# Kernel tuning notes

Measured on AMD Instinct MI355X. Metric: run time of the kernel, lower is better.

The kernel has to match this reference:

```python
import jax, jax.numpy as jnp
import numpy as np

N, E, IN_DIM, HID = 50000, 800000, 128, 128
HEADS, HEAD_DIM = 4, HID // 4
LN_EPS = 1e-5
NEG_SLOPE = 0.2


def layer_norm(x, g, b):
    m = jnp.mean(x, axis=-1, keepdims=True)
    v = jnp.mean(jnp.square(x - m), axis=-1, keepdims=True)
    return (x - m) / jnp.sqrt(v + LN_EPS) * g + b


def setup_inputs() -> dict:
    key = jax.random.key(0)
    ks = jax.random.split(key, 24)
    s = lambda k, shape, scale=0.05: jax.random.normal(k, shape, dtype=jnp.float32) * scale
    inp = {
        "x": jax.random.normal(ks[0], (N, IN_DIM), dtype=jnp.float32),
        "edge_weight": jax.random.uniform(ks[1], (E,), dtype=jnp.float32),
        # GATConv params
        "gat_w": s(ks[2], (IN_DIM, HID)),          # lin weight (transposed), bias=False in PyG lin
        "att_src": s(ks[3], (HEADS, HEAD_DIM)),
        "att_dst": s(ks[4], (HEADS, HEAD_DIM)),
        "gat_b": s(ks[5], (HID,)),                 # GATConv bias (concat=True -> size heads*out)
        # predictive-coding branch: spectral_norm(Linear) + LayerNorm + ReLU
        "pc_w": s(ks[6], (HID, HID)),
        "pc_b": s(ks[7], (HID,)),
        "pc_g": jnp.ones((HID,), jnp.float32),
        "pc_bb": jnp.zeros((HID,), jnp.float32),
        # MGF branch: Linear -> (Linear + LayerNorm + ReLU)
        "mgf_w": s(ks[8], (HID, HID)),
        "mgf_b": s(ks[9], (HID,)),
        "sym_w": s(ks[10], (HID, HID)),
        "sym_b": s(ks[11], (HID,)),
        "sym_g": jnp.ones((HID,), jnp.float32),
        "sym_bb": jnp.zeros((HID,), jnp.float32),
        # output projection + final norm
        "out_w": s(ks[12], (3 * HID, HID)),
        "out_b": s(ks[13], (HID,)),
        "norm_g": jnp.ones((HID,), jnp.float32),
        "norm_b": jnp.zeros((HID,), jnp.float32),
        # int-typed graph structure (batch is unused by the layer, kept for fidelity)
        "edge_index": jax.random.randint(ks[14], (2, E), 0, N, dtype=jnp.int64),
        "batch": jax.random.randint(ks[15], (N,), 0, 782, dtype=jnp.int64),
    }
    return inp


def gat_conv(x, edge_index, gat_w, att_src, att_dst, gat_b):
    # PyG GATConv (eval mode, dropout off), add_self_loops=True, concat=True
    loops = jnp.arange(N, dtype=edge_index.dtype)
    src = jnp.concatenate([edge_index[0], loops])
    dst = jnp.concatenate([edge_index[1], loops])
    xp = (x @ gat_w).reshape(N, HEADS, HEAD_DIM)          # [N,H,C]
    a_src = jnp.sum(xp * att_src, axis=-1)                 # [N,H]
    a_dst = jnp.sum(xp * att_dst, axis=-1)                 # [N,H]
    e = jax.nn.leaky_relu(a_src[src] + a_dst[dst], NEG_SLOPE)  # [E+N,H]
    # segment softmax over incoming edges of each destination node
    m = jax.ops.segment_max(e, dst, num_segments=N)        # [N,H]
    e_exp = jnp.exp(e - m[dst])
    denom = jax.ops.segment_sum(e_exp, dst, num_segments=N)
    alpha = e_exp / (denom[dst] + 1e-16)                   # [E+N,H]
    msg = xp[src] * alpha[:, :, None]                      # [E+N,H,C]
    out = jax.ops.segment_sum(msg, dst, num_segments=N)    # [N,H,C]
    return out.reshape(N, HID) + gat_b


def reference(x, edge_weight, gat_w, att_src, att_dst, gat_b,
              pc_w, pc_b, pc_g, pc_bb,
              mgf_w, mgf_b, sym_w, sym_b, sym_g, sym_bb,
              out_w, out_b, norm_g, norm_b,
              edge_index, batch):
    h_gat = gat_conv(x, edge_index, gat_w, att_src, att_dst, gat_b)
    feats = [h_gat]
    # predictive coding: spectral-normalized linear -> LN -> ReLU
    sigma = jnp.linalg.norm(pc_w, ord=2)
    h_pred = jax.nn.relu(layer_norm(h_gat @ (pc_w / sigma) + pc_b, pc_g, pc_bb))
    feats.append(h_pred)
    # MGF: mgf_proj then symbiotic (Linear -> LN -> ReLU)
    h_mgf = jax.nn.relu(layer_norm((h_gat @ mgf_w + mgf_b) @ sym_w + sym_b, sym_g, sym_bb))
    feats.append(h_mgf)
    h_comb = jnp.concatenate(feats, axis=-1)               # [N, 3*HID]
    h_out = h_comb @ out_w + out_b
    return layer_norm(h_out, norm_g, norm_b)
```

## Files before the change

kernel.cpp:

```cpp
#include <hip/hip_runtime.h>
#include <cstddef>

#define HID 128
#define NEG_SLOPE 0.2f
#define LN_EPS 1e-5f

typedef float floatx4 __attribute__((ext_vector_type(4)));
typedef short bf16x8 __attribute__((ext_vector_type(8)));
typedef int intx4 __attribute__((ext_vector_type(4)));
typedef unsigned short u16;
typedef unsigned int u32;

#define MFMA(a, b, c) __builtin_amdgcn_mfma_f32_16x16x32_bf16((a), (b), (c), 0, 0, 0)

__device__ __forceinline__ u16 f2bf(float f) {
  union { float f; unsigned u; } v; v.f = f;
  unsigned r = v.u + 0x7FFF + ((v.u >> 16) & 1);
  return (u16)(r >> 16);
}
__device__ __forceinline__ float bf2f(u16 s) {
  union { unsigned u; float f; } v; v.u = ((unsigned)s) << 16;
  return v.f;
}

__global__ void build_G_zero(const float* __restrict__ W, float* __restrict__ G,
                             int* __restrict__ cnt, int N) {
  const int b = blockIdx.x;
  if (b < HID) {
    int i = b, j = threadIdx.x;
    float s = 0.f;
    for (int k = 0; k < HID; ++k) s = fmaf(W[k*HID + i], W[k*HID + j], s);
    G[i*HID + j] = s;
  } else {
    int i = (b - HID) * 128 + threadIdx.x;
    if (i < N) cnt[i] = 0;
  }
}

__global__ void mat_sq(const float* __restrict__ A, float* __restrict__ C) {
  int i = blockIdx.x, j = threadIdx.x;
  float s = 0.f;
  for (int k = 0; k < HID; ++k) s = fmaf(A[i*HID + k], A[k*HID + j], s);
  C[i*HID + j] = s;
}

__global__ __launch_bounds__(256) void power_iter_lds(
    const float* __restrict__ H, float* __restrict__ out_inv_sigma) {
  __shared__ __align__(16) float Hl[128 * 132];
  __shared__ __align__(16) float v[132];
  __shared__ float ybuf[256];
  __shared__ float red[8];
  const int tid = threadIdx.x;
  {
    const float4* H4 = (const float4*)H;
    float4* Hl4 = (float4*)Hl;
    #pragma unroll
    for (int idx = tid; idx < 128*32; idx += 256) {
      int r = idx >> 5, c = idx & 31;
      Hl4[r*33 + c] = H4[idx];
    }
  }
  if (tid < 128) v[tid] = 1.0f + 0.001f * (float)tid;
  __syncthreads();
  const int j = tid & 127, half = tid >> 7;
  float rho = 0.f;
  for (int it = 0; it < 20; ++it) {
    const float4* hrow = (const float4*)(Hl + j*132 + half*64);
    const float4* vrow = (const float4*)(v) + half*16;
    float y = 0.f;
    #pragma unroll
    for (int q = 0; q < 16; ++q) {
      float4 hq = hrow[q];
      float4 vq = vrow[q];
      y += hq.x*vq.x + hq.y*vq.y + hq.z*vq.z + hq.w*vq.w;
    }
    ybuf[tid] = y;
    __syncthreads();
    float yj = 0.f, vy = 0.f, yy = 0.f;
    if (tid < 128) {
      yj = ybuf[tid] + ybuf[tid + 128];
      vy = v[tid] * yj;
      yy = yj * yj;
    }
    #pragma unroll
    for (int m = 1; m < 64; m <<= 1) { vy += __shfl_xor(vy, m); yy += __shfl_xor(yy, m); }
    if ((tid & 63) == 0) { red[tid>>6] = vy; red[4 + (tid>>6)] = yy; }
    __syncthreads();
    float vyT = red[0] + red[1] + red[2] + red[3];
    float yyT = red[4] + red[5] + red[6] + red[7];
    rho = vyT;
    if (tid < 128) v[tid] = yj * rsqrtf(yyT);
    __syncthreads();
  }
  if (tid == 0) {
    out_inv_sigma[0] = 1.0f / sqrtf(sqrtf(rho));
  }
}

__global__ void prep_all(const float* __restrict__ pc_w, const float* __restrict__ sigma_inv,
                         const float* __restrict__ mgf_w, const float* __restrict__ mgf_b,
                         const float* __restrict__ sym_w, const float* __restrict__ sym_b,
                         const float* __restrict__ out_w,
                         u16* __restrict__ W1t, u16* __restrict__ W2t,
                         u16* __restrict__ Wot, float* __restrict__ bias2) {
  const int b = blockIdx.x;
  const int j = threadIdx.x;
  if (b < HID) {
    float s = 0.f;
    for (int m = 0; m < HID; ++m) s = fmaf(mgf_w[b*HID + m], sym_w[m*HID + j], s);
    W2t[j*HID + b] = f2bf(s);
  } else if (b == HID) {
    float s = sym_b[j];
    for (int m = 0; m < HID; ++m) s = fmaf(mgf_b[m], sym_w[m*HID + j], s);
    bias2[j] = s;
  } else if (b == HID + 1) {
    float sc = sigma_inv[0];
    for (int k = 0; k < HID; ++k) W1t[j*HID + k] = f2bf(pc_w[k*HID + j] * sc);
  } else {
    int p = b - (HID + 2);
    for (int k = 0; k < HID; ++k)
      Wot[p*HID*HID + j*HID + k] = f2bf(out_w[(size_t)(p*HID + k)*HID + j]);
  }
}

__global__ __launch_bounds__(256) void xp_mfma(
    const float* __restrict__ x, const float* __restrict__ W,
    const float* __restrict__ att_src, const float* __restrict__ att_dst,
    u16* __restrict__ xp, float* __restrict__ a_src, float* __restrict__ a_dst,
    int nrows)
{
  __shared__ u16 Wt[128 * 136];
  const int tid = threadIdx.x;
  {
    const float4* W4 = (const float4*)W;
    #pragma unroll
    for (int i = 0; i < 16; ++i) {
      int i4 = tid + i*256;
      int k = i4 >> 5, n4 = i4 & 31;
      float4 w = W4[i4];
      Wt[(n4*4+0)*136 + k] = f2bf(w.x);
      Wt[(n4*4+1)*136 + k] = f2bf(w.y);
      Wt[(n4*4+2)*136 + k] = f2bf(w.z);
      Wt[(n4*4+3)*136 + k] = f2bf(w.w);
    }
  }
  __syncthreads();
  const int lane = tid & 63, wave = tid >> 6;
  const int lr = lane & 15, lg = lane >> 4;
  const int rowbase = blockIdx.x*128 + wave*32;

  bf16x8 a[2][4];
  #pragma unroll
  for (int rf = 0; rf < 2; ++rf) {
    int row = min(rowbase + rf*16 + lr, nrows-1);
    const float* p = x + (size_t)row*HID + lg*8;
    #pragma unroll
    for (int kc = 0; kc < 4; ++kc) {
      float4 q0 = *(const float4*)(p + kc*32);
      float4 q1 = *(const float4*)(p + kc*32 + 4);
      union { bf16x8 v; u16 s[8]; } u;
      u.s[0]=f2bf(q0.x); u.s[1]=f2bf(q0.y); u.s[2]=f2bf(q0.z); u.s[3]=f2bf(q0.w);
      u.s[4]=f2bf(q1.x); u.s[5]=f2bf(q1.y); u.s[6]=f2bf(q1.z); u.s[7]=f2bf(q1.w);
      a[rf][kc] = u.v;
    }
  }
  floatx4 acc[2][8];
  #pragma unroll
  for (int rf = 0; rf < 2; ++rf)
    #pragma unroll
    for (int cf = 0; cf < 8; ++cf) acc[rf][cf] = (floatx4){0,0,0,0};
  #pragma unroll
  for (int kc = 0; kc < 4; ++kc)
    #pragma unroll
    for (int cf = 0; cf < 8; ++cf) {
      bf16x8 b = *(const bf16x8*)&Wt[(cf*16+lr)*136 + kc*32 + lg*8];
      acc[0][cf] = MFMA(a[0][kc], b, acc[0][cf]);
      acc[1][cf] = MFMA(a[1][kc], b, acc[1][cf]);
    }
  float asv[8], adv[8];
  #pragma unroll
  for (int cf = 0; cf < 8; ++cf) {
    asv[cf] = att_src[cf*16 + lr];
    adv[cf] = att_dst[cf*16 + lr];
  }
  #pragma unroll
  for (int rf = 0; rf < 2; ++rf) {
    #pragma unroll
    for (int j = 0; j < 4; ++j) {
      int row = rowbase + rf*16 + lg*4 + j;
      if (row < nrows) {
        #pragma unroll
        for (int cf = 0; cf < 8; ++cf)
          xp[(size_t)row*HID + cf*16 + lr] = f2bf(acc[rf][cf][j]);
      }
      #pragma unroll
      for (int h = 0; h < 4; ++h) {
        float ps = acc[rf][2*h][j]*asv[2*h] + acc[rf][2*h+1][j]*asv[2*h+1];
        float pd = acc[rf][2*h][j]*adv[2*h] + acc[rf][2*h+1][j]*adv[2*h+1];
        #pragma unroll
        for (int m = 1; m < 16; m <<= 1) { ps += __shfl_xor(ps, m); pd += __shfl_xor(pd, m); }
        if (lr == 0 && row < nrows) {
          a_src[(size_t)row*4 + h] = ps;
          a_dst[(size_t)row*4 + h] = pd;
        }
      }
    }
  }
}

__global__ __launch_bounds__(256) void tail_fused(
    const u16* __restrict__ A,
    const u16* __restrict__ W1t, const float* __restrict__ b1,
    const float* __restrict__ g1, const float* __restrict__ bb1,
    const u16* __restrict__ W2t, const float* __restrict__ b2,
    const float* __restrict__ g2, const float* __restrict__ bb2,
    const u16* __restrict__ Wot,
    const float* __restrict__ out_b,
    const float* __restrict__ norm_g, const float* __restrict__ norm_b,
    float* __restrict__ Cout, int nrows)
{
  __shared__ u16 Wbuf[128 * 136];
  __shared__ u16 T[64 * 136];
  const int tid = threadIdx.x;
  const int lane = tid & 63, wave = tid >> 6;
  const int lr = lane & 15, lg = lane >> 4;
  const int rowbase = blockIdx.x * 64;

  int arow = min(rowbase + wave*16 + lr, nrows-1);
  const u16* ap = A + (size_t)arow*HID + lg*8;
  bf16x8 a0 = *(const bf16x8*)(ap);
  bf16x8 a1 = *(const bf16x8*)(ap + 32);
  bf16x8 a2 = *(const bf16x8*)(ap + 64);
  bf16x8 a3 = *(const bf16x8*)(ap + 96);

  bf16x8 st[8];
  auto loadW = [&](const u16* Wsrc) {
    #pragma unroll
    for (int i = 0; i < 8; ++i)
      st[i] = *(const bf16x8*)(Wsrc + (size_t)(tid + i*256) * 8);
  };
  auto writeW = [&]() {
    #pragma unroll
    for (int i = 0; i < 8; ++i) {
      int c = tid + i*256;
      *(bf16x8*)&Wbuf[(c >> 4)*136 + (c & 15)*8] = st[i];
    }
  };
  auto gemmW = [&](floatx4* acc, bf16x8 x0, bf16x8 x1, bf16x8 x2, bf16x8 x3) {
    #pragma unroll
    for (int cf = 0; cf < 8; ++cf) {
      const u16* wb = &Wbuf[(cf*16+lr)*136 + lg*8];
      acc[cf] = MFMA(x0, *(const bf16x8*)(wb),       acc[cf]);
      acc[cf] = MFMA(x1, *(const bf16x8*)(wb + 32),  acc[cf]);
      acc[cf] = MFMA(x2, *(const bf16x8*)(wb + 64),  acc[cf]);
      acc[cf] = MFMA(x3, *(const bf16x8*)(wb + 96),  acc[cf]);
    }
  };
  auto epiT = [&](floatx4* acc, const float* bias, const float* lng, const float* lnb) {
    #pragma unroll
    for (int j = 0; j < 4; ++j) {
      float vv[8]; float s1 = 0.f, s2 = 0.f;
      #pragma unroll
      for (int cf = 0; cf < 8; ++cf) {
        vv[cf] = acc[cf][j] + bias[cf*16 + lr];
        s1 += vv[cf]; s2 += vv[cf]*vv[cf];
      }
      #pragma unroll
      for (int m = 1; m < 16; m <<= 1) { s1 += __shfl_xor(s1, m); s2 += __shfl_xor(s2, m); }
      float mean = s1 * (1.0f/128.0f);
      float var  = s2 * (1.0f/128.0f) - mean*mean;
      float rstd = rsqrtf(var + LN_EPS);
      int lrow = wave*16 + lg*4 + j;
      #pragma unroll
      for (int cf = 0; cf < 8; ++cf) {
        float o = fmaxf((vv[cf]-mean)*rstd*lng[cf*16+lr] + lnb[cf*16+lr], 0.f);
        T[lrow*136 + cf*16 + lr] = f2bf(o);
      }
    }
  };

  floatx4 accO[8];
  #pragma unroll
  for (int cf = 0; cf < 8; ++cf) accO[cf] = (floatx4){0,0,0,0};

  loadW(W1t);
  writeW(); __syncthreads();
  loadW(Wot + (size_t)1*HID*HID);
  {
    floatx4 accT[8];
    #pragma unroll
    for (int cf = 0; cf < 8; ++cf) accT[cf] = (floatx4){0,0,0,0};
    gemmW(accT, a0, a1, a2, a3);
    epiT(accT, b1, g1, bb1);
  }
  __syncthreads();
  writeW(); __syncthreads();
  loadW(W2t);
  {
    const u16* tp = &T[(wave*16 + lr)*136 + lg*8];
    bf16x8 t0 = *(const bf16x8*)(tp);
    bf16x8 t1 = *(const bf16x8*)(tp + 32);
    bf16x8 t2 = *(const bf16x8*)(tp + 64);
    bf16x8 t3 = *(const bf16x8*)(tp + 96);
    gemmW(accO, t0, t1, t2, t3);
  }
  __syncthreads();
  writeW(); __syncthreads();
  loadW(Wot + (size_t)2*HID*HID);
  {
    floatx4 accT[8];
    #pragma unroll
    for (int cf = 0; cf < 8; ++cf) accT[cf] = (floatx4){0,0,0,0};
    gemmW(accT, a0, a1, a2, a3);
    epiT(accT, b2, g2, bb2);
  }
  __syncthreads();
  writeW(); __syncthreads();
  loadW(Wot);
  {
    const u16* tp = &T[(wave*16 + lr)*136 + lg*8];
    bf16x8 t0 = *(const bf16x8*)(tp);
    bf16x8 t1 = *(const bf16x8*)(tp + 32);
    bf16x8 t2 = *(const bf16x8*)(tp + 64);
    bf16x8 t3 = *(const bf16x8*)(tp + 96);
    gemmW(accO, t0, t1, t2, t3);
  }
  __syncthreads();
  writeW(); __syncthreads();
  gemmW(accO, a0, a1, a2, a3);

  #pragma unroll
  for (int j = 0; j < 4; ++j) {
    float vv[8]; float s1 = 0.f, s2 = 0.f;
    #pragma unroll
    for (int cf = 0; cf < 8; ++cf) {
      vv[cf] = accO[cf][j] + out_b[cf*16 + lr];
      s1 += vv[cf]; s2 += vv[cf]*vv[cf];
    }
    #pragma unroll
    for (int m = 1; m < 16; m <<= 1) { s1 += __shfl_xor(s1, m); s2 += __shfl_xor(s2, m); }
    float mean = s1 * (1.0f/128.0f);
    float var  = s2 * (1.0f/128.0f) - mean*mean;
    float rstd = rsqrtf(var + LN_EPS);
    int row = rowbase + wave*16 + lg*4 + j;
    if (row < nrows) {
      #pragma unroll
      for (int cf = 0; cf < 8; ++cf)
        Cout[(size_t)row*HID + cf*16 + lr] = (vv[cf]-mean)*rstd*norm_g[cf*16+lr] + norm_b[cf*16+lr];
    }
  }
}

__global__ __launch_bounds__(256) void hist_rank(
    const int* __restrict__ ei, int E, int N,
    int* __restrict__ cnt, int* __restrict__ rank) {
  const int E4 = E >> 2;
  const intx4* dst4 = (const intx4*)(ei + (size_t)E);
  intx4* rank4 = (intx4*)rank;
  const int stride = gridDim.x * 256;
  for (int i4 = blockIdx.x*256 + threadIdx.x; i4 < E4; i4 += stride) {
    intx4 d4 = __builtin_nontemporal_load(&dst4[i4]);
    intx4 r;
    r.x = ((unsigned)d4.x < (unsigned)N) ? atomicAdd(&cnt[d4.x], 1) : 0;
    r.y = ((unsigned)d4.y < (unsigned)N) ? atomicAdd(&cnt[d4.y], 1) : 0;
    r.z = ((unsigned)d4.z < (unsigned)N) ? atomicAdd(&cnt[d4.z], 1) : 0;
    r.w = ((unsigned)d4.w < (unsigned)N) ? atomicAdd(&cnt[d4.w], 1) : 0;
    rank4[i4] = r;
  }
}

__global__ void hist_rank_tail(const int* __restrict__ ei, int E, int N,
                               int* __restrict__ cnt, int* __restrict__ rank) {
  int t = threadIdx.x;
  int E4 = E >> 2;
  int ntail = E & 3;
  if (t < ntail) {
    int idx = (E4 << 2) + t;
    int d = ei[(size_t)E + idx];
    rank[idx] = ((unsigned)d < (unsigned)N) ? atomicAdd(&cnt[d], 1) : 0;
  }
}

__global__ void scan_local(const int* __restrict__ cnt, int* __restrict__ row_ptr,
                           int* __restrict__ blk_tot, int N) {
  __shared__ int sd[1024];
  int tid = threadIdx.x;
  int i = blockIdx.x * 1024 + tid;
  int v = (i < N) ? cnt[i] : 0;
  sd[tid] = v;
  __syncthreads();
  for (int off = 1; off < 1024; off <<= 1) {
    int t = (tid >= off) ? sd[tid - off] : 0;
    __syncthreads();
    sd[tid] += t;
    __syncthreads();
  }
  if (i < N) row_ptr[i] = sd[tid] - v;
  if (tid == 1023) blk_tot[blockIdx.x] = sd[1023];
}

__global__ void scan_apply2(int* __restrict__ row_ptr,
                            const int* __restrict__ blk_tot, int N, int nb) {
  __shared__ int s_off;
  const int tid = threadIdx.x;
  const int bid = blockIdx.x;
  if (tid < 64) {
    int carry = 0;
    for (int base = 0; base < nb; base += 64) {
      int i = base + tid;
      int v = (i < nb) ? blk_tot[i] : 0;
      int inc = v;
      #pragma unroll
      for (int m = 1; m < 64; m <<= 1) {
        int t = __shfl_up(inc, m);
        if (tid >= m) inc += t;
      }
      if (i == bid) s_off = carry + inc - v;
      int tot = __shfl(inc, 63);
      carry += tot;
    }
    if (bid == 0 && tid == 0) row_ptr[N] = carry;
  }
  __syncthreads();
  int i = bid * 1024 + tid;
  if (i < N) row_ptr[i] += s_off;
}

__global__ __launch_bounds__(256) void fill_rank(
    const int* __restrict__ ei, int E, int N,
    const int* __restrict__ row_ptr, const int* __restrict__ rank,
    int* __restrict__ csr_src) {
  const int E4 = E >> 2;
  const intx4* src4v = (const intx4*)ei;
  const intx4* dst4v = (const intx4*)(ei + (size_t)E);
  const intx4* rank4 = (const intx4*)rank;
  const int stride = gridDim.x * 256;
  for (int i4 = blockIdx.x*256 + threadIdx.x; i4 < E4; i4 += stride) {
    intx4 d4 = __builtin_nontemporal_load(&dst4v[i4]);
    intx4 s4 = __builtin_nontemporal_load(&src4v[i4]);
    intx4 r4 = __builtin_nontemporal_load(&rank4[i4]);
    if ((unsigned)d4.x < (unsigned)N && (unsigned)s4.x < (unsigned)N)
      csr_src[row_ptr[d4.x] + r4.x] = s4.x;
    if ((unsigned)d4.y < (unsigned)N && (unsigned)s4.y < (unsigned)N)
      csr_src[row_ptr[d4.y] + r4.y] = s4.y;
    if ((unsigned)d4.z < (unsigned)N && (unsigned)s4.z < (unsigned)N)
      csr_src[row_ptr[d4.z] + r4.z] = s4.z;
    if ((unsigned)d4.w < (unsigned)N && (unsigned)s4.w < (unsigned)N)
      csr_src[row_ptr[d4.w] + r4.w] = s4.w;
  }
}

__global__ void fill_rank_tail(const int* __restrict__ ei, int E, int N,
                               const int* __restrict__ row_ptr, const int* __restrict__ rank,
                               int* __restrict__ csr_src) {
  int t = threadIdx.x;
  int E4 = E >> 2;
  int ntail = E & 3;
  if (t < ntail) {
    int idx = (E4 << 2) + t;
    int d = ei[(size_t)E + idx];
    int s = ei[idx];
    if ((unsigned)d < (unsigned)N && (unsigned)s < (unsigned)N)
      csr_src[row_ptr[d] + rank[idx]] = s;
  }
}

__global__ __launch_bounds__(64) void gat_aggregate(
    const u16* __restrict__ xp, const float* __restrict__ a_src,
    const float* __restrict__ a_dst, const int* __restrict__ row_ptr,
    const int* __restrict__ csr_src, const float* __restrict__ gat_b,
    u16* __restrict__ h_gat, int N)
{
  const int d = blockIdx.x;
  const int lane = threadIdx.x;
  const int hh = lane >> 4;
  const int c0 = lane * 2;
  const int beg = row_ptr[d], end = row_ptr[d+1];

  const float ad = a_dst[(size_t)d*4 + hh];
  float e0 = a_src[(size_t)d*4 + hh] + ad;
  e0 = (e0 > 0.f) ? e0 : NEG_SLOPE * e0;
  float w0 = __expf(e0);
  u32 xv = *(const u32*)(xp + (size_t)d*HID + c0);
  float acc0 = w0 * bf2f((u16)(xv & 0xFFFF));
  float acc1 = w0 * bf2f((u16)(xv >> 16));
  float den = w0;

  int i = beg;
  for (; i + 4 <= end; i += 4) {
    int s0 = csr_src[i+0], s1 = csr_src[i+1], s2 = csr_src[i+2], s3 = csr_src[i+3];
    float eA = a_src[(size_t)s0*4 + hh] + ad;
    float eB = a_src[(size_t)s1*4 + hh] + ad;
    float eC = a_src[(size_t)s2*4 + hh] + ad;
    float eD = a_src[(size_t)s3*4 + hh] + ad;
    eA = (eA > 0.f) ? eA : NEG_SLOPE * eA;
    eB = (eB > 0.f) ? eB : NEG_SLOPE * eB;
    eC = (eC > 0.f) ? eC : NEG_SLOPE * eC;
    eD = (eD > 0.f) ? eD : NEG_SLOPE * eD;
    float wA = __expf(eA), wB = __expf(eB), wC = __expf(eC), wD = __expf(eD);
    u32 xA = *(const u32*)(xp + (size_t)s0*HID + c0);
    u32 xB = *(const u32*)(xp + (size_t)s1*HID + c0);
    u32 xC = *(const u32*)(xp + (size_t)s2*HID + c0);
    u32 xD = *(const u32*)(xp + (size_t)s3*HID + c0);
    acc0 = fmaf(wA, bf2f((u16)(xA & 0xFFFF)), acc0);
    acc1 = fmaf(wA, bf2f((u16)(xA >> 16)),    acc1);
    acc0 = fmaf(wB, bf2f((u16)(xB & 0xFFFF)), acc0);
    acc1 = fmaf(wB, bf2f((u16)(xB >> 16)),    acc1);
    acc0 = fmaf(wC, bf2f((u16)(xC & 0xFFFF)), acc0);
    acc1 = fmaf(wC, bf2f((u16)(xC >> 16)),    acc1);
    acc0 = fmaf(wD, bf2f((u16)(xD & 0xFFFF)), acc0);
    acc1 = fmaf(wD, bf2f((u16)(xD >> 16)),    acc1);
    den += (wA + wB) + (wC + wD);
  }
  for (; i < end; ++i) {
    int s = csr_src[i];
    float e = a_src[(size_t)s*4 + hh] + ad;
    e = (e > 0.f) ? e : NEG_SLOPE * e;
    float w = __expf(e);
    u32 xw = *(const u32*)(xp + (size_t)s*HID + c0);
    acc0 = fmaf(w, bf2f((u16)(xw & 0xFFFF)), acc0);
    acc1 = fmaf(w, bf2f((u16)(xw >> 16)),    acc1);
    den += w;
  }
  float inv = 1.0f / (den + 1e-16f);
  float o0 = acc0 * inv + gat_b[c0];
  float o1 = acc1 * inv + gat_b[c0 + 1];
  u32 pack = (u32)f2bf(o0) | ((u32)f2bf(o1) << 16);
  *(u32*)(h_gat + (size_t)d*HID + c0) = pack;
}

extern "C" void kernel_launch(void* const* d_in, const int* in_sizes, int n_in,
                              void* d_out, int out_size, void* d_ws, size_t ws_size,
                              hipStream_t stream) {
  const float* x       = (const float*)d_in[0];
  const float* gat_w   = (const float*)d_in[2];
  const float* att_src = (const float*)d_in[3];
  const float* att_dst = (const float*)d_in[4];
  const float* gat_b   = (const float*)d_in[5];
  const float* pc_w    = (const float*)d_in[6];
  const float* pc_b    = (const float*)d_in[7];
  const float* pc_g    = (const float*)d_in[8];
  const float* pc_bb   = (const float*)d_in[9];
  const float* mgf_w   = (const float*)d_in[10];
  const float* mgf_b   = (const float*)d_in[11];
  const float* sym_w   = (const float*)d_in[12];
  const float* sym_b   = (const float*)d_in[13];
  const float* sym_g   = (const float*)d_in[14];
  const float* sym_bb  = (const float*)d_in[15];
  const float* out_w   = (const float*)d_in[16];
  const float* out_b   = (const float*)d_in[17];
  const float* norm_g  = (const float*)d_in[18];
  const float* norm_b  = (const float*)d_in[19];
  const int*   ei      = (const int*)d_in[20];

  const int N = in_sizes[0] / HID;
  const int E = in_sizes[1];
  const int NB = (N + 1023) / 1024;
  const int NZB = (N + 127) / 128;

  char* ws = (char*)d_ws;
  size_t off = 0;
  auto alloc = [&](size_t bytes) -> void* {
    void* p = ws + off;
    off += (bytes + 255) & ~(size_t)255;
    return p;
  };
  u16*   xp       = (u16*)alloc((size_t)N * HID * 2);
  u16*   h_gat    = (u16*)alloc((size_t)N * HID * 2);
  float* a_src    = (float*)alloc((size_t)N * 4 * 4);
  float* a_dst    = (float*)alloc((size_t)N * 4 * 4);
  int*   cnt      = (int*)alloc((size_t)N * 4);
  int*   row_ptr  = (int*)alloc((size_t)(N + 1) * 4);
  int*   erank    = (int*)alloc((size_t)E * 4);
  int*   blk_tot  = (int*)alloc(256 * 4);
  int*   csr_src  = (int*)alloc((size_t)E * 4);
  float* G        = (float*)alloc(HID * HID * 4);
  float* Hm       = (float*)alloc(HID * HID * 4);
  float* bias2    = (float*)alloc(HID * 4);
  float* sigma_inv= (float*)alloc(256);
  u16*   W1t      = (u16*)alloc(HID * HID * 2);
  u16*   W2t      = (u16*)alloc(HID * HID * 2);
  u16*   Wot      = (u16*)alloc(3 * HID * HID * 2);

  const int ntiles = (N + 127) / 128;
  const int ntiles64 = (N + 63) / 64;

  build_G_zero<<<HID + NZB, HID, 0, stream>>>(pc_w, G, cnt, N);
  mat_sq<<<HID, HID, 0, stream>>>(G, Hm);
  power_iter_lds<<<1, 256, 0, stream>>>(Hm, sigma_inv);

  prep_all<<<HID + 5, HID, 0, stream>>>(pc_w, sigma_inv, mgf_w, mgf_b, sym_w, sym_b,
                                        out_w, W1t, W2t, Wot, bias2);

  xp_mfma<<<ntiles, 256, 0, stream>>>(x, gat_w, att_src, att_dst, xp, a_src, a_dst, N);

  hist_rank<<<1024, 256, 0, stream>>>(ei, E, N, cnt, erank);
  if (E & 3) hist_rank_tail<<<1, 64, 0, stream>>>(ei, E, N, cnt, erank);
  scan_local<<<NB, 1024, 0, stream>>>(cnt, row_ptr, blk_tot, N);
  scan_apply2<<<NB, 1024, 0, stream>>>(row_ptr, blk_tot, N, NB);
  fill_rank<<<1024, 256, 0, stream>>>(ei, E, N, row_ptr, erank, csr_src);
  if (E & 3) fill_rank_tail<<<1, 64, 0, stream>>>(ei, E, N, row_ptr, erank, csr_src);

  gat_aggregate<<<N, 64, 0, stream>>>(xp, a_src, a_dst, row_ptr, csr_src,
                                      gat_b, h_gat, N);

  tail_fused<<<ntiles64, 256, 0, stream>>>(h_gat,
      W1t, pc_b, pc_g, pc_bb,
      W2t, bias2, sym_g, sym_bb,
      Wot, out_b, norm_g, norm_b,
      (float*)d_out, N);
}
```

Measured before the change: 186.1 us.

## Merge independent prep, projection and CSR-build kernels into fewer launches

Fuses the weight-prep chain (Gram matrix, squaring, power iteration, weight packing) with the independent xp projection and the CSR construction stages by giving each stage its own range of block indices inside shared kernels. The launch count drops from about eleven to five plus a memset, so small serial kernels overlap with the larger ones. The cost is heavier per-kernel resource footprints, such as LDS for the xp tiles being reserved in every block, and branch-divergent block roles.

Measured after the change: 166.3 us. 1.12x faster.

```diff
diff --git a/kernel.cpp b/kernel.cpp
--- a/kernel.cpp
+++ b/kernel.cpp
@@ -23,445 +23,292 @@
   return v.f;
 }
 
-__global__ void build_G_zero(const float* __restrict__ W, float* __restrict__ G,
-                             int* __restrict__ cnt, int N) {
+__global__ __launch_bounds__(256) void K_front(
+    const float* __restrict__ x, const float* __restrict__ W,
+    const float* __restrict__ att_src, const float* __restrict__ att_dst,
+    u16* __restrict__ xp, float* __restrict__ a_src, float* __restrict__ a_dst,
+    int nrows, int ntXP,
+    const float* __restrict__ pc_w, float* __restrict__ G,
+    const int* __restrict__ ei, int E, int N,
+    int* __restrict__ cnt, int* __restrict__ rank)
+{
+  __shared__ u16 Wt[128 * 136];
   const int b = blockIdx.x;
-  if (b < HID) {
-    int i = b, j = threadIdx.x;
+  const int tid = threadIdx.x;
+
+  if (b < ntXP) {
+    {
+      const float4* W4 = (const float4*)W;
+      #pragma unroll
+      for (int i = 0; i < 16; ++i) {
+        int i4 = tid + i*256;
+        int k = i4 >> 5, n4 = i4 & 31;
+        float4 w = W4[i4];
+        Wt[(n4*4+0)*136 + k] = f2bf(w.x);
+        Wt[(n4*4+1)*136 + k] = f2bf(w.y);
+        Wt[(n4*4+2)*136 + k] = f2bf(w.z);
+        Wt[(n4*4+3)*136 + k] = f2bf(w.w);
+      }
+    }
+    __syncthreads();
+    const int lane = tid & 63, wave = tid >> 6;
+    const int lr = lane & 15, lg = lane >> 4;
+    const int rowbase = b*128 + wave*32;
+
+    bf16x8 a[2][4];
+    #pragma unroll
+    for (int rf = 0; rf < 2; ++rf) {
+      int row = min(rowbase + rf*16 + lr, nrows-1);
+      const float* p = x + (size_t)row*HID + lg*8;
+      #pragma unroll
+      for (int kc = 0; kc < 4; ++kc) {
+        float4 q0 = *(const float4*)(p + kc*32);
+        float4 q1 = *(const float4*)(p + kc*32 + 4);
+        union { bf16x8 v; u16 s[8]; } u;
+        u.s[0]=f2bf(q0.x); u.s[1]=f2bf(q0.y); u.s[2]=f2bf(q0.z); u.s[3]=f2bf(q0.w);
+        u.s[4]=f2bf(q1.x); u.s[5]=f2bf(q1.y); u.s[6]=f2bf(q1.z); u.s[7]=f2bf(q1.w);
+        a[rf][kc] = u.v;
+      }
+    }
+    floatx4 acc[2][8];
+    #pragma unroll
+    for (int rf = 0; rf < 2; ++rf)
+      #pragma unroll
+      for (int cf = 0; cf < 8; ++cf) acc[rf][cf] = (floatx4){0,0,0,0};
+    #pragma unroll
+    for (int kc = 0; kc < 4; ++kc)
+      #pragma unroll
+      for (int cf = 0; cf < 8; ++cf) {
+        bf16x8 bb = *(const bf16x8*)&Wt[(cf*16+lr)*136 + kc*32 + lg*8];
+        acc[0][cf] = MFMA(a[0][kc], bb, acc[0][cf]);
+        acc[1][cf] = MFMA(a[1][kc], bb, acc[1][cf]);
+      }
+    float asv[8], adv[8];
+    #pragma unroll
+    for (int cf = 0; cf < 8; ++cf) {
+      asv[cf] = att_src[cf*16 + lr];
+      adv[cf] = att_dst[cf*16 + lr];
+    }
+    #pragma unroll
+    for (int rf = 0; rf < 2; ++rf) {
+      #pragma unroll
+      for (int j = 0; j < 4; ++j) {
+        int row = rowbase + rf*16 + lg*4 + j;
+        if (row < nrows) {
+          #pragma unroll
+          for (int cf = 0; cf < 8; ++cf)
+            xp[(size_t)row*HID + cf*16 + lr] = f2bf(acc[rf][cf][j]);
+        }
+        #pragma unroll
+        for (int h = 0; h < 4; ++h) {
+          float ps = acc[rf][2*h][j]*asv[2*h] + acc[rf][2*h+1][j]*asv[2*h+1];
+          float pd = acc[rf][2*h][j]*adv[2*h] + acc[rf][2*h+1][j]*adv[2*h+1];
+          #pragma unroll
+          for (int m = 1; m < 16; m <<= 1) { ps += __shfl_xor(ps, m); pd += __shfl_xor(pd, m); }
+          if (lr == 0 && row < nrows) {
+            a_src[(size_t)row*4 + h] = ps;
+            a_dst[(size_t)row*4 + h] = pd;
+          }
+        }
+      }
+    }
+  } else if (b < ntXP + 64) {
+    int i = (b - ntXP)*2 + (tid >> 7);
+    int j = tid & 127;
     float s = 0.f;
-    for (int k = 0; k < HID; ++k) s = fmaf(W[k*HID + i], W[k*HID + j], s);
+    for (int k = 0; k < HID; ++k) s = fmaf(pc_w[k*HID + i], pc_w[k*HID + j], s);
     G[i*HID + j] = s;
   } else {
-    int i = (b - HID) * 128 + threadIdx.x;
-    if (i < N) cnt[i] = 0;
-  }
-}
-
-__global__ void mat_sq(const float* __restrict__ A, float* __restrict__ C) {
-  int i = blockIdx.x, j = threadIdx.x;
-  float s = 0.f;
-  for (int k = 0; k < HID; ++k) s = fmaf(A[i*HID + k], A[k*HID + j], s);
-  C[i*HID + j] = s;
-}
-
-__global__ __launch_bounds__(256) void power_iter_lds(
-    const float* __restrict__ H, float* __restrict__ out_inv_sigma) {
+    const int vb = b - (ntXP + 64);
+    const int nhb = gridDim.x - (ntXP + 64);
+    const int E4 = E >> 2;
+    const intx4* dst4 = (const intx4*)(ei + (size_t)E);
+    intx4* rank4 = (intx4*)rank;
+    const int stride = nhb * 256;
+    for (int i4 = vb*256 + tid; i4 < E4; i4 += stride) {
+      intx4 d4 = __builtin_nontemporal_load(&dst4[i4]);
+      intx4 r;
+      r.x = ((unsigned)d4.x < (unsigned)N) ? atomicAdd(&cnt[d4.x], 1) : 0;
+      r.y = ((unsigned)d4.y < (unsigned)N) ? atomicAdd(&cnt[d4.y], 1) : 0;
+      r.z = ((unsigned)d4.z < (unsigned)N) ? atomicAdd(&cnt[d4.z], 1) : 0;
+      r.w = ((unsigned)d4.w < (unsigned)N) ? atomicAdd(&cnt[d4.w], 1) : 0;
+      rank4[i4] = r;
+    }
+    if (b == ntXP + 64 && tid < (E & 3)) {
+      int idx = (E4 << 2) + tid;
+      int d = ei[(size_t)E + idx];
+      rank[idx] = ((unsigned)d < (unsigned)N) ? atomicAdd(&cnt[d], 1) : 0;
+    }
+  }
+}
+
+__global__ __launch_bounds__(1024) void K_scan(
+    const int* __restrict__ cnt, int* __restrict__ row_ptr,
+    int* __restrict__ blk_tot, int N, int NB,
+    const float* __restrict__ G, float* __restrict__ Hm)
+{
+  __shared__ int sd[1024];
+  const int b = blockIdx.x;
+  const int tid = threadIdx.x;
+  if (b < NB) {
+    int i = b * 1024 + tid;
+    int v = (i < N) ? cnt[i] : 0;
+    sd[tid] = v;
+    __syncthreads();
+    for (int off = 1; off < 1024; off <<= 1) {
+      int t = (tid >= off) ? sd[tid - off] : 0;
+      __syncthreads();
+      sd[tid] += t;
+      __syncthreads();
+    }
+    if (i < N) row_ptr[i] = sd[tid] - v;
+    if (tid == 1023) blk_tot[b] = sd[1023];
+  } else {
+    int i = (b - NB)*8 + (tid >> 7);
+    int j = tid & 127;
+    float s = 0.f;
+    for (int k = 0; k < HID; ++k) s = fmaf(G[i*HID + k], G[k*HID + j], s);
+    Hm[i*HID + j] = s;
+  }
+}
+
+__global__ __launch_bounds__(256) void K_apply(
+    int* __restrict__ row_ptr, const int* __restrict__ blk_tot, int N, int NB,
+    const float* __restrict__ H, float* __restrict__ out_inv_sigma)
+{
   __shared__ __align__(16) float Hl[128 * 132];
   __shared__ __align__(16) float v[132];
   __shared__ float ybuf[256];
   __shared__ float red[8];
+  __shared__ int s_off;
+  const int b = blockIdx.x;
   const int tid = threadIdx.x;
-  {
-    const float4* H4 = (const float4*)H;
-    float4* Hl4 = (float4*)Hl;
-    #pragma unroll
-    for (int idx = tid; idx < 128*32; idx += 256) {
-      int r = idx >> 5, c = idx & 31;
-      Hl4[r*33 + c] = H4[idx];
-    }
-  }
-  if (tid < 128) v[tid] = 1.0f + 0.001f * (float)tid;
-  __syncthreads();
-  const int j = tid & 127, half = tid >> 7;
-  float rho = 0.f;
-  for (int it = 0; it < 20; ++it) {
-    const float4* hrow = (const float4*)(Hl + j*132 + half*64);
-    const float4* vrow = (const float4*)(v) + half*16;
-    float y = 0.f;
-    #pragma unroll
-    for (int q = 0; q < 16; ++q) {
-      float4 hq = hrow[q];
-      float4 vq = vrow[q];
-      y += hq.x*vq.x + hq.y*vq.y + hq.z*vq.z + hq.w*vq.w;
-    }
-    ybuf[tid] = y;
+
+  if (b < NB) {
+    if (tid < 64) {
+      int carry = 0;
+      for (int base = 0; base < NB; base += 64) {
+        int i = base + tid;
+        int vv = (i < NB) ? blk_tot[i] : 0;
+        int inc = vv;
+        #pragma unroll
+        for (int m = 1; m < 64; m <<= 1) {
+          int t = __shfl_up(inc, m);
+          if (tid >= m) inc += t;
+        }
+        if (i == b) s_off = carry + inc - vv;
+        int tot = __shfl(inc, 63);
+        carry += tot;
+      }
+      if (b == 0 && tid == 0) row_ptr[N] = carry;
+    }
     __syncthreads();
-    float yj = 0.f, vy = 0.f, yy = 0.f;
-    if (tid < 128) {
-      yj = ybuf[tid] + ybuf[tid + 128];
-      vy = v[tid] * yj;
-      yy = yj * yj;
-    }
-    #pragma unroll
-    for (int m = 1; m < 64; m <<= 1) { vy += __shfl_xor(vy, m); yy += __shfl_xor(yy, m); }
-    if ((tid & 63) == 0) { red[tid>>6] = vy; red[4 + (tid>>6)] = yy; }
+    int lim = min(N, (b + 1) * 1024);
+    for (int i = b * 1024 + tid; i < lim; i += 256) row_ptr[i] += s_off;
+  } else {
+    {
+      const float4* H4 = (const float4*)H;
+      float4* Hl4 = (float4*)Hl;
+      #pragma unroll
+      for (int idx = tid; idx < 128*32; idx += 256) {
+        int r = idx >> 5, c = idx & 31;
+        Hl4[r*33 + c] = H4[idx];
+      }
+    }
+    if (tid < 128) v[tid] = 1.0f + 0.001f * (float)tid;
     __syncthreads();
-    float vyT = red[0] + red[1] + red[2] + red[3];
-    float yyT = red[4] + red[5] + red[6] + red[7];
-    rho = vyT;
-    if (tid < 128) v[tid] = yj * rsqrtf(yyT);
-    __syncthreads();
-  }
-  if (tid == 0) {
-    out_inv_sigma[0] = 1.0f / sqrtf(sqrtf(rho));
-  }
-}
-
-__global__ void prep_all(const float* __restrict__ pc_w, const float* __restrict__ sigma_inv,
-                         const float* __restrict__ mgf_w, const float* __restrict__ mgf_b,
-                         const float* __restrict__ sym_w, const float* __restrict__ sym_b,
-                         const float* __restrict__ out_w,
-                         u16* __restrict__ W1t, u16* __restrict__ W2t,
-                         u16* __restrict__ Wot, float* __restrict__ bias2) {
-  const int b = blockIdx.x;
-  const int j = threadIdx.x;
-  if (b < HID) {
-    float s = 0.f;
-    for (int m = 0; m < HID; ++m) s = fmaf(mgf_w[b*HID + m], sym_w[m*HID + j], s);
-    W2t[j*HID + b] = f2bf(s);
-  } else if (b == HID) {
-    float s = sym_b[j];
-    for (int m = 0; m < HID; ++m) s = fmaf(mgf_b[m], sym_w[m*HID + j], s);
-    bias2[j] = s;
-  } else if (b == HID + 1) {
-    float sc = sigma_inv[0];
-    for (int k = 0; k < HID; ++k) W1t[j*HID + k] = f2bf(pc_w[k*HID + j] * sc);
-  } else {
-    int p = b - (HID + 2);
-    for (int k = 0; k < HID; ++k)
-      Wot[p*HID*HID + j*HID + k] = f2bf(out_w[(size_t)(p*HID + k)*HID + j]);
-  }
-}
-
-__global__ __launch_bounds__(256) void xp_mfma(
-    const float* __restrict__ x, const float* __restrict__ W,
-    const float* __restrict__ att_src, const float* __restrict__ att_dst,
-    u16* __restrict__ xp, float* __restrict__ a_src, float* __restrict__ a_dst,
-    int nrows)
-{
-  __shared__ u16 Wt[128 * 136];
-  const int tid = threadIdx.x;
-  {
-    const float4* W4 = (const float4*)W;
-    #pragma unroll
-    for (int i = 0; i < 16; ++i) {
-      int i4 = tid + i*256;
-      int k = i4 >> 5, n4 = i4 & 31;
-      float4 w = W4[i4];
-      Wt[(n4*4+0)*136 + k] = f2bf(w.x);
-      Wt[(n4*4+1)*136 + k] = f2bf(w.y);
-      Wt[(n4*4+2)*136 + k] = f2bf(w.z);
-      Wt[(n4*4+3)*136 + k] = f2bf(w.w);
-    }
-  }
-  __syncthreads();
-  const int lane = tid & 63, wave = tid >> 6;
-  const int lr = lane & 15, lg = lane >> 4;
-  const int rowbase = blockIdx.x*128 + wave*32;
-
-  bf16x8 a[2][4];
-  #pragma unroll
-  for (int rf = 0; rf < 2; ++rf) {
-    int row = min(rowbase + rf*16 + lr, nrows-1);
-    const float* p = x + (size_t)row*HID + lg*8;
-    #pragma unroll
-    for (int kc = 0; kc < 4; ++kc) {
-      float4 q0 = *(const float4*)(p + kc*32);
-      float4 q1 = *(const float4*)(p + kc*32 + 4);
-      union { bf16x8 v; u16 s[8]; } u;
-      u.s[0]=f2bf(q0.x); u.s[1]=f2bf(q0.y); u.s[2]=f2bf(q0.z); u.s[3]=f2bf(q0.w);
-      u.s[4]=f2bf(q1.x); u.s[5]=f2bf(q1.y); u.s[6]=f2bf(q1.z); u.s[7]=f2bf(q1.w);
-      a[rf][kc] = u.v;
-    }
-  }
-  floatx4 acc[2][8];
-  #pragma unroll
-  for (int rf = 0; rf < 2; ++rf)
-    #pragma unroll
-    for (int cf = 0; cf < 8; ++cf) acc[rf][cf] = (floatx4){0,0,0,0};
-  #pragma unroll
-  for (int kc = 0; kc < 4; ++kc)
-    #pragma unroll
-    for (int cf = 0; cf < 8; ++cf) {
-      bf16x8 b = *(const bf16x8*)&Wt[(cf*16+lr)*136 + kc*32 + lg*8];
-      acc[0][cf] = MFMA(a[0][kc], b, acc[0][cf]);
-      acc[1][cf] = MFMA(a[1][kc], b, acc[1][cf]);
-    }
-  float asv[8], adv[8];
-  #pragma unroll
-  for (int cf = 0; cf < 8; ++cf) {
-    asv[cf] = att_src[cf*16 + lr];
-    adv[cf] = att_dst[cf*16 + lr];
-  }
-  #pragma unroll
-  for (int rf = 0; rf < 2; ++rf) {
-    #pragma unroll
-    for (int j = 0; j < 4; ++j) {
-      int row = rowbase + rf*16 + lg*4 + j;
-      if (row < nrows) {
-        #pragma unroll
-        for (int cf = 0; cf < 8; ++cf)
-          xp[(size_t)row*HID + cf*16 + lr] = f2bf(acc[rf][cf][j]);
-      }
-      #pragma unroll
-      for (int h = 0; h < 4; ++h) {
-        float ps = acc[rf][2*h][j]*asv[2*h] + acc[rf][2*h+1][j]*asv[2*h+1];
-        float pd = acc[rf][2*h][j]*adv[2*h] + acc[rf][2*h+1][j]*adv[2*h+1];
-        #pragma unroll
-        for (int m = 1; m < 16; m <<= 1) { ps += __shfl_xor(ps, m); pd += __shfl_xor(pd, m); }
-        if (lr == 0 && row < nrows) {
-          a_src[(size_t)row*4 + h] = ps;
-          a_dst[(size_t)row*4 + h] = pd;
-        }
-      }
-    }
-  }
-}
-
-__global__ __launch_bounds__(256) void tail_fused(
-    const u16* __restrict__ A,
-    const u16* __restrict__ W1t, const float* __restrict__ b1,
-    const float* __restrict__ g1, const float* __restrict__ bb1,
-    const u16* __restrict__ W2t, const float* __restrict__ b2,
-    const float* __restrict__ g2, const float* __restrict__ bb2,
-    const u16* __restrict__ Wot,
-    const float* __restrict__ out_b,
-    const float* __restrict__ norm_g, const float* __restrict__ norm_b,
-    float* __restrict__ Cout, int nrows)
-{
-  __shared__ u16 Wbuf[128 * 136];
-  __shared__ u16 T[64 * 136];
-  const int tid = threadIdx.x;
-  const int lane = tid & 63, wave = tid >> 6;
-  const int lr = lane & 15, lg = lane >> 4;
-  const int rowbase = blockIdx.x * 64;
-
-  int arow = min(rowbase + wave*16 + lr, nrows-1);
-  const u16* ap = A + (size_t)arow*HID + lg*8;
-  bf16x8 a0 = *(const bf16x8*)(ap);
-  bf16x8 a1 = *(const bf16x8*)(ap + 32);
-  bf16x8 a2 = *(const bf16x8*)(ap + 64);
-  bf16x8 a3 = *(const bf16x8*)(ap + 96);
-
-  bf16x8 st[8];
-  auto loadW = [&](const u16* Wsrc) {
-    #pragma unroll
-    for (int i = 0; i < 8; ++i)
-      st[i] = *(const bf16x8*)(Wsrc + (size_t)(tid + i*256) * 8);
-  };
-  auto writeW = [&]() {
-    #pragma unroll
-    for (int i = 0; i < 8; ++i) {
-      int c = tid + i*256;
-      *(bf16x8*)&Wbuf[(c >> 4)*136 + (c & 15)*8] = st[i];
-    }
-  };
-  auto gemmW = [&](floatx4* acc, bf16x8 x0, bf16x8 x1, bf16x8 x2, bf16x8 x3) {
-    #pragma unroll
-    for (int cf = 0; cf < 8; ++cf) {
-      const u16* wb = &Wbuf[(cf*16+lr)*136 + lg*8];
-      acc[cf] = MFMA(x0, *(const bf16x8*)(wb),       acc[cf]);
-      acc[cf] = MFMA(x1, *(const bf16x8*)(wb + 32),  acc[cf]);
-      acc[cf] = MFMA(x2, *(const bf16x8*)(wb + 64),  acc[cf]);
-      acc[cf] = MFMA(x3, *(const bf16x8*)(wb + 96),  acc[cf]);
-    }
-  };
-  auto epiT = [&](floatx4* acc, const float* bias, const float* lng, const float* lnb) {
-    #pragma unroll
-    for (int j = 0; j < 4; ++j) {
-      float vv[8]; float s1 = 0.f, s2 = 0.f;
-      #pragma unroll
-      for (int cf = 0; cf < 8; ++cf) {
-        vv[cf] = acc[cf][j] + bias[cf*16 + lr];
-        s1 += vv[cf]; s2 += vv[cf]*vv[cf];
-      }
-      #pragma unroll
-      for (int m = 1; m < 16; m <<= 1) { s1 += __shfl_xor(s1, m); s2 += __shfl_xor(s2, m); }
-      float mean = s1 * (1.0f/128.0f);
-      float var  = s2 * (1.0f/128.0f) - mean*mean;
-      float rstd = rsqrtf(var + LN_EPS);
-      int lrow = wave*16 + lg*4 + j;
-      #pragma unroll
-      for (int cf = 0; cf < 8; ++cf) {
-        float o = fmaxf((vv[cf]-mean)*rstd*lng[cf*16+lr] + lnb[cf*16+lr], 0.f);
-        T[lrow*136 + cf*16 + lr] = f2bf(o);
-      }
-    }
-  };
-
-  floatx4 accO[8];
-  #pragma unroll
-  for (int cf = 0; cf < 8; ++cf) accO[cf] = (floatx4){0,0,0,0};
-
-  loadW(W1t);
-  writeW(); __syncthreads();
-  loadW(Wot + (size_t)1*HID*HID);
-  {
-    floatx4 accT[8];
-    #pragma unroll
-    for (int cf = 0; cf < 8; ++cf) accT[cf] = (floatx4){0,0,0,0};
-    gemmW(accT, a0, a1, a2, a3);
-    epiT(accT, b1, g1, bb1);
-  }
-  __syncthreads();
-  writeW(); __syncthreads();
-  loadW(W2t);
-  {
-    const u16* tp = &T[(wave*16 + lr)*136 + lg*8];
-    bf16x8 t0 = *(const bf16x8*)(tp);
-    bf16x8 t1 = *(const bf16x8*)(tp + 32);
-    bf16x8 t2 = *(const bf16x8*)(tp + 64);
-    bf16x8 t3 = *(const bf16x8*)(tp + 96);
-    gemmW(accO, t0, t1, t2, t3);
-  }
-  __syncthreads();
-  writeW(); __syncthreads();
-  loadW(Wot + (size_t)2*HID*HID);
-  {
-    floatx4 accT[8];
-    #pragma unroll
-    for (int cf = 0; cf < 8; ++cf) accT[cf] = (floatx4){0,0,0,0};
-    gemmW(accT, a0, a1, a2, a3);
-    epiT(accT, b2, g2, bb2);
-  }
-  __syncthreads();
-  writeW(); __syncthreads();
-  loadW(Wot);
-  {
-    const u16* tp = &T[(wave*16 + lr)*136 + lg*8];
-    bf16x8 t0 = *(const bf16x8*)(tp);
-    bf16x8 t1 = *(const bf16x8*)(tp + 32);
-    bf16x8 t2 = *(const bf16x8*)(tp + 64);
-    bf16x8 t3 = *(const bf16x8*)(tp + 96);
-    gemmW(accO, t0, t1, t2, t3);
-  }
-  __syncthreads();
-  writeW(); __syncthreads();
-  gemmW(accO, a0, a1, a2, a3);
-
-  #pragma unroll
-  for (int j = 0; j < 4; ++j) {
-    float vv[8]; float s1 = 0.f, s2 = 0.f;
-    #pragma unroll
-    for (int cf = 0; cf < 8; ++cf) {
-      vv[cf] = accO[cf][j] + out_b[cf*16 + lr];
-      s1 += vv[cf]; s2 += vv[cf]*vv[cf];
-    }
-    #pragma unroll
-    for (int m = 1; m < 16; m <<= 1) { s1 += __shfl_xor(s1, m); s2 += __shfl_xor(s2, m); }
-    float mean = s1 * (1.0f/128.0f);
-    float var  = s2 * (1.0f/128.0f) - mean*mean;
-    float rstd = rsqrtf(var + LN_EPS);
-    int row = rowbase + wave*16 + lg*4 + j;
-    if (row < nrows) {
-      #pragma unroll
-      for (int cf = 0; cf < 8; ++cf)
-        Cout[(size_t)row*HID + cf*16 + lr] = (vv[cf]-mean)*rstd*norm_g[cf*16+lr] + norm_b[cf*16+lr];
-    }
-  }
-}
-
-__global__ __launch_bounds__(256) void hist_rank(
-    const int* __restrict__ ei, int E, int N,
-    int* __restrict__ cnt, int* __restrict__ rank) {
-  const int E4 = E >> 2;
-  const intx4* dst4 = (const intx4*)(ei + (size_t)E);
-  intx4* rank4 = (intx4*)rank;
-  const int stride = gridDim.x * 256;
-  for (int i4 = blockIdx.x*256 + threadIdx.x; i4 < E4; i4 += stride) {
-    intx4 d4 = __builtin_nontemporal_load(&dst4[i4]);
-    intx4 r;
-    r.x = ((unsigned)d4.x < (unsigned)N) ? atomicAdd(&cnt[d4.x], 1) : 0;
-    r.y = ((unsigned)d4.y < (unsigned)N) ? atomicAdd(&cnt[d4.y], 1) : 0;
-    r.z = ((unsigned)d4.z < (unsigned)N) ? atomicAdd(&cnt[d4.z], 1) : 0;
-    r.w = ((unsigned)d4.w < (unsigned)N) ? atomicAdd(&cnt[d4.w], 1) : 0;
-    rank4[i4] = r;
-  }
-}
-
-__global__ void hist_rank_tail(const int* __restrict__ ei, int E, int N,
-                               int* __restrict__ cnt, int* __restrict__ rank) {
-  int t = threadIdx.x;
-  int E4 = E >> 2;
-  int ntail = E & 3;
-  if (t < ntail) {
-    int idx = (E4 << 2) + t;
-    int d = ei[(size_t)E + idx];
-    rank[idx] = ((unsigned)d < (unsigned)N) ? atomicAdd(&cnt[d], 1) : 0;
-  }
-}
-
-__global__ void scan_local(const int* __restrict__ cnt, int* __restrict__ row_ptr,
-                           int* __restrict__ blk_tot, int N) {
-  __shared__ int sd[1024];
-  int tid = threadIdx.x;
-  int i = blockIdx.x * 1024 + tid;
-  int v = (i < N) ? cnt[i] : 0;
-  sd[tid] = v;
-  __syncthreads();
-  for (int off = 1; off < 1024; off <<= 1) {
-    int t = (tid >= off) ? sd[tid - off] : 0;
-    __syncthreads();
-    sd[tid] += t;
-    __syncthreads();
-  }
-  if (i < N) row_ptr[i] = sd[tid] - v;
-  if (tid == 1023) blk_tot[blockIdx.x] = sd[1023];
-}
-
-__global__ void scan_apply2(int* __restrict__ row_ptr,
-                            const int* __restrict__ blk_tot, int N, int nb) {
-  __shared__ int s_off;
-  const int tid = threadIdx.x;
-  const int bid = blockIdx.x;
-  if (tid < 64) {
-    int carry = 0;
-    for (int base = 0; base < nb; base += 64) {
-      int i = base + tid;
-      int v = (i < nb) ? blk_tot[i] : 0;
-      int inc = v;
-      #pragma unroll
-      for (int m = 1; m < 64; m <<= 1) {
-        int t = __shfl_up(inc, m);
-        if (tid >= m) inc += t;
-      }
-      if (i == bid) s_off = carry + inc - v;
-      int tot = __shfl(inc, 63);
-      carry += tot;
-    }
-    if (bid == 0 && tid == 0) row_ptr[N] = carry;
-  }
-  __syncthreads();
-  int i = bid * 1024 + tid;
-  if (i < N) row_ptr[i] += s_off;
-}
-
-__global__ __launch_bounds__(256) void fill_rank(
+    const int j = tid & 127, half = tid >> 7;
+    float rho = 0.f;
+    for (int it = 0; it < 20; ++it) {
+      const float4* hrow = (const float4*)(Hl + j*132 + half*64);
+      const float4* vrow = (const float4*)(v) + half*16;
+      float y = 0.f;
+      #pragma unroll
+      for (int q = 0; q < 16; ++q) {
+        float4 hq = hrow[q];
+        float4 vq = vrow[q];
+        y += hq.x*vq.x + hq.y*vq.y + hq.z*vq.z + hq.w*vq.w;
+      }
+      ybuf[tid] = y;
+      __syncthreads();
+      float yj = 0.f, vy = 0.f, yy = 0.f;
+      if (tid < 128) {
+        yj = ybuf[tid] + ybuf[tid + 128];
+        vy = v[tid] * yj;
+        yy = yj * yj;
+      }
+      #pragma unroll
+      for (int m = 1; m < 64; m <<= 1) { vy += __shfl_xor(vy, m); yy += __shfl_xor(yy, m); }
+      if ((tid & 63) == 0) { red[tid>>6] = vy; red[4 + (tid>>6)] = yy; }
+      __syncthreads();
+      float vyT = red[0] + red[1] + red[2] + red[3];
+      float yyT = red[4] + red[5] + red[6] + red[7];
+      rho = vyT;
+      if (tid < 128) v[tid] = yj * rsqrtf(yyT);
+      __syncthreads();
+    }
+    if (tid == 0) out_inv_sigma[0] = 1.0f / sqrtf(sqrtf(rho));
+  }
+}
+
+__global__ __launch_bounds__(256) void K_fill(
     const int* __restrict__ ei, int E, int N,
     const int* __restrict__ row_ptr, const int* __restrict__ rank,
-    int* __restrict__ csr_src) {
-  const int E4 = E >> 2;
-  const intx4* src4v = (const intx4*)ei;
-  const intx4* dst4v = (const intx4*)(ei + (size_t)E);
-  const intx4* rank4 = (const intx4*)rank;
-  const int stride = gridDim.x * 256;
-  for (int i4 = blockIdx.x*256 + threadIdx.x; i4 < E4; i4 += stride) {
-    intx4 d4 = __builtin_nontemporal_load(&dst4v[i4]);
-    intx4 s4 = __builtin_nontemporal_load(&src4v[i4]);
-    intx4 r4 = __builtin_nontemporal_load(&rank4[i4]);
-    if ((unsigned)d4.x < (unsigned)N && (unsigned)s4.x < (unsigned)N)
-      csr_src[row_ptr[d4.x] + r4.x] = s4.x;
-    if ((unsigned)d4.y < (unsigned)N && (unsigned)s4.y < (unsigned)N)
-      csr_src[row_ptr[d4.y] + r4.y] = s4.y;
-    if ((unsigned)d4.z < (unsigned)N && (unsigned)s4.z < (unsigned)N)
-      csr_src[row_ptr[d4.z] + r4.z] = s4.z;
-    if ((unsigned)d4.w < (unsigned)N && (unsigned)s4.w < (unsigned)N)
-      csr_src[row_ptr[d4.w] + r4.w] = s4.w;
-  }
-}
-
-__global__ void fill_rank_tail(const int* __restrict__ ei, int E, int N,
-                               const int* __restrict__ row_ptr, const int* __restrict__ rank,
-                               int* __restrict__ csr_src) {
-  int t = threadIdx.x;
-  int E4 = E >> 2;
-  int ntail = E & 3;
-  if (t < ntail) {
-    int idx = (E4 << 2) + t;
-    int d = ei[(size_t)E + idx];
-    int s = ei[idx];
-    if ((unsigned)d < (unsigned)N && (unsigned)s < (unsigned)N)
-      csr_src[row_ptr[d] + rank[idx]] = s;
+    int* __restrict__ csr_src,
+    const float* __restrict__ pc_w, const float* __restrict__ sigma_inv,
+    const float* __restrict__ mgf_w, const float* __restrict__ mgf_b,
+    const float* __restrict__ sym_w, const float* __restrict__ sym_b,
+    const float* __restrict__ out_w,
+    u16* __restrict__ W1t, u16* __restrict__ W2t,
+    u16* __restrict__ Wot, float* __restrict__ bias2)
+{
+  const int b = blockIdx.x;
+  const int tid = threadIdx.x;
+  if (b < 1024) {
+    const int E4 = E >> 2;
+    const intx4* src4v = (const intx4*)ei;
+    const intx4* dst4v = (const intx4*)(ei + (size_t)E);
+    const intx4* rank4 = (const intx4*)rank;
+    const int stride = 1024 * 256;
+    for (int i4 = b*256 + tid; i4 < E4; i4 += stride) {
+      intx4 d4 = __builtin_nontemporal_load(&dst4v[i4]);
+      intx4 s4 = __builtin_nontemporal_load(&src4v[i4]);
+      intx4 r4 = __builtin_nontemporal_load(&rank4[i4]);
+      if ((unsigned)d4.x < (unsigned)N && (unsigned)s4.x < (unsigned)N)
+        csr_src[row_ptr[d4.x] + r4.x] = s4.x;
+      if ((unsigned)d4.y < (unsigned)N && (unsigned)s4.y < (unsigned)N)
+        csr_src[row_ptr[d4.y] + r4.y] = s4.y;
+      if ((unsigned)d4.z < (unsigned)N && (unsigned)s4.z < (unsigned)N)
+        csr_src[row_ptr[d4.z] + r4.z] = s4.z;
+      if ((unsigned)d4.w < (unsigned)N && (unsigned)s4.w < (unsigned)N)
+        csr_src[row_ptr[d4.w] + r4.w] = s4.w;
+    }
+    if (b == 0 && tid < (E & 3)) {
+      int idx = ((E >> 2) << 2) + tid;
+      int d = ei[(size_t)E + idx];
+      int s = ei[idx];
+      if ((unsigned)d < (unsigned)N && (unsigned)s < (unsigned)N)
+        csr_src[row_ptr[d] + rank[idx]] = s;
+    }
+  } else if (tid < 128) {
+    const int bb = b - 1024;
+    const int j = tid;
+    if (bb < HID) {
+      float s = 0.f;
+      for (int m = 0; m < HID; ++m) s = fmaf(mgf_w[bb*HID + m], sym_w[m*HID + j], s);
+      W2t[j*HID + bb] = f2bf(s);
+    } else if (bb == HID) {
+      float s = sym_b[j];
+      for (int m = 0; m < HID; ++m) s = fmaf(mgf_b[m], sym_w[m*HID + j], s);
+      bias2[j] = s;
+    } else if (bb == HID + 1) {
+      float sc = sigma_inv[0];
+      for (int k = 0; k < HID; ++k) W1t[j*HID + k] = f2bf(pc_w[k*HID + j] * sc);
+    } else {
+      int p = bb - (HID + 2);
+      for (int k = 0; k < HID; ++k)
+        Wot[p*HID*HID + j*HID + k] = f2bf(out_w[(size_t)(p*HID + k)*HID + j]);
+    }
   }
 }
 
@@ -529,6 +376,149 @@
   *(u32*)(h_gat + (size_t)d*HID + c0) = pack;
 }
 
+__global__ __launch_bounds__(256) void tail_fused(
+    const u16* __restrict__ A,
+    const u16* __restrict__ W1t, const float* __restrict__ b1,
+    const float* __restrict__ g1, const float* __restrict__ bb1,
+    const u16* __restrict__ W2t, const float* __restrict__ b2,
+    const float* __restrict__ g2, const float* __restrict__ bb2,
+    const u16* __restrict__ Wot,
+    const float* __restrict__ out_b,
+    const float* __restrict__ norm_g, const float* __restrict__ norm_b,
+    float* __restrict__ Cout, int nrows)
+{
+  __shared__ u16 Wbuf[128 * 136];
+  __shared__ u16 T[64 * 136];
+  const int tid = threadIdx.x;
+  const int lane = tid & 63, wave = tid >> 6;
+  const int lr = lane & 15, lg = lane >> 4;
+  const int rowbase = blockIdx.x * 64;
+
+  int arow = min(rowbase + wave*16 + lr, nrows-1);
+  const u16* ap = A + (size_t)arow*HID + lg*8;
+  bf16x8 a0 = *(const bf16x8*)(ap);
+  bf16x8 a1 = *(const bf16x8*)(ap + 32);
+  bf16x8 a2 = *(const bf16x8*)(ap + 64);
+  bf16x8 a3 = *(const bf16x8*)(ap + 96);
+
+  bf16x8 st[8];
+  auto loadW = [&](const u16* Wsrc) {
+    #pragma unroll
+    for (int i = 0; i < 8; ++i)
+      st[i] = *(const bf16x8*)(Wsrc + (size_t)(tid + i*256) * 8);
+  };
+  auto writeW = [&]() {
+    #pragma unroll
+    for (int i = 0; i < 8; ++i) {
+      int c = tid + i*256;
+      *(bf16x8*)&Wbuf[(c >> 4)*136 + (c & 15)*8] = st[i];
+    }
+  };
+  auto gemmW = [&](floatx4* acc, bf16x8 x0, bf16x8 x1, bf16x8 x2, bf16x8 x3) {
+    #pragma unroll
+    for (int cf = 0; cf < 8; ++cf) {
+      const u16* wb = &Wbuf[(cf*16+lr)*136 + lg*8];
+      acc[cf] = MFMA(x0, *(const bf16x8*)(wb),       acc[cf]);
+      acc[cf] = MFMA(x1, *(const bf16x8*)(wb + 32),  acc[cf]);
+      acc[cf] = MFMA(x2, *(const bf16x8*)(wb + 64),  acc[cf]);
+      acc[cf] = MFMA(x3, *(const bf16x8*)(wb + 96),  acc[cf]);
+    }
+  };
+  auto epiT = [&](floatx4* acc, const float* bias, const float* lng, const float* lnb) {
+    #pragma unroll
+    for (int j = 0; j < 4; ++j) {
+      float vv[8]; float s1 = 0.f, s2 = 0.f;
+      #pragma unroll
+      for (int cf = 0; cf < 8; ++cf) {
+        vv[cf] = acc[cf][j] + bias[cf*16 + lr];
+        s1 += vv[cf]; s2 += vv[cf]*vv[cf];
+      }
+      #pragma unroll
+      for (int m = 1; m < 16; m <<= 1) { s1 += __shfl_xor(s1, m); s2 += __shfl_xor(s2, m); }
+      float mean = s1 * (1.0f/128.0f);
+      float var  = s2 * (1.0f/128.0f) - mean*mean;
+      float rstd = rsqrtf(var + LN_EPS);
+      int lrow = wave*16 + lg*4 + j;
+      #pragma unroll
+      for (int cf = 0; cf < 8; ++cf) {
+        float o = fmaxf((vv[cf]-mean)*rstd*lng[cf*16+lr] + lnb[cf*16+lr], 0.f);
+        T[lrow*136 + cf*16 + lr] = f2bf(o);
+      }
+    }
+  };
+
+  floatx4 accO[8];
+  #pragma unroll
+  for (int cf = 0; cf < 8; ++cf) accO[cf] = (floatx4){0,0,0,0};
+
+  loadW(W1t);
+  writeW(); __syncthreads();
+  loadW(Wot + (size_t)1*HID*HID);
+  {
+    floatx4 accT[8];
+    #pragma unroll
+    for (int cf = 0; cf < 8; ++cf) accT[cf] = (floatx4){0,0,0,0};
+    gemmW(accT, a0, a1, a2, a3);
+    epiT(accT, b1, g1, bb1);
+  }
+  __syncthreads();
+  writeW(); __syncthreads();
+  loadW(W2t);
+  {
+    const u16* tp = &T[(wave*16 + lr)*136 + lg*8];
+    bf16x8 t0 = *(const bf16x8*)(tp);
+    bf16x8 t1 = *(const bf16x8*)(tp + 32);
+    bf16x8 t2 = *(const bf16x8*)(tp + 64);
+    bf16x8 t3 = *(const bf16x8*)(tp + 96);
+    gemmW(accO, t0, t1, t2, t3);
+  }
+  __syncthreads();
+  writeW(); __syncthreads();
+  loadW(Wot + (size_t)2*HID*HID);
+  {
+    floatx4 accT[8];
+    #pragma unroll
+    for (int cf = 0; cf < 8; ++cf) accT[cf] = (floatx4){0,0,0,0};
+    gemmW(accT, a0, a1, a2, a3);
+    epiT(accT, b2, g2, bb2);
+  }
+  __syncthreads();
+  writeW(); __syncthreads();
+  loadW(Wot);
+  {
+    const u16* tp = &T[(wave*16 + lr)*136 + lg*8];
+    bf16x8 t0 = *(const bf16x8*)(tp);
+    bf16x8 t1 = *(const bf16x8*)(tp + 32);
+    bf16x8 t2 = *(const bf16x8*)(tp + 64);
+    bf16x8 t3 = *(const bf16x8*)(tp + 96);
+    gemmW(accO, t0, t1, t2, t3);
+  }
+  __syncthreads();
+  writeW(); __syncthreads();
+  gemmW(accO, a0, a1, a2, a3);
+
+  #pragma unroll
+  for (int j = 0; j < 4; ++j) {
+    float vv[8]; float s1 = 0.f, s2 = 0.f;
+    #pragma unroll
+    for (int cf = 0; cf < 8; ++cf) {
+      vv[cf] = accO[cf][j] + out_b[cf*16 + lr];
+      s1 += vv[cf]; s2 += vv[cf]*vv[cf];
+    }
+    #pragma unroll
+    for (int m = 1; m < 16; m <<= 1) { s1 += __shfl_xor(s1, m); s2 += __shfl_xor(s2, m); }
+    float mean = s1 * (1.0f/128.0f);
+    float var  = s2 * (1.0f/128.0f) - mean*mean;
+    float rstd = rsqrtf(var + LN_EPS);
+    int row = rowbase + wave*16 + lg*4 + j;
+    if (row < nrows) {
+      #pragma unroll
+      for (int cf = 0; cf < 8; ++cf)
+        Cout[(size_t)row*HID + cf*16 + lr] = (vv[cf]-mean)*rstd*norm_g[cf*16+lr] + norm_b[cf*16+lr];
+    }
+  }
+}
+
 extern "C" void kernel_launch(void* const* d_in, const int* in_sizes, int n_in,
                               void* d_out, int out_size, void* d_ws, size_t ws_size,
                               hipStream_t stream) {
@@ -556,7 +546,6 @@
   const int N = in_sizes[0] / HID;
   const int E = in_sizes[1];
   const int NB = (N + 1023) / 1024;
-  const int NZB = (N + 127) / 128;
 
   char* ws = (char*)d_ws;
   size_t off = 0;
@@ -582,24 +571,23 @@
   u16*   W2t      = (u16*)alloc(HID * HID * 2);
   u16*   Wot      = (u16*)alloc(3 * HID * HID * 2);
 
-  const int ntiles = (N + 127) / 128;
+  const int ntXP = (N + 127) / 128;
   const int ntiles64 = (N + 63) / 64;
 
-  build_G_zero<<<HID + NZB, HID, 0, stream>>>(pc_w, G, cnt, N);
-  mat_sq<<<HID, HID, 0, stream>>>(G, Hm);
-  power_iter_lds<<<1, 256, 0, stream>>>(Hm, sigma_inv);
-
-  prep_all<<<HID + 5, HID, 0, stream>>>(pc_w, sigma_inv, mgf_w, mgf_b, sym_w, sym_b,
-                                        out_w, W1t, W2t, Wot, bias2);
-
-  xp_mfma<<<ntiles, 256, 0, stream>>>(x, gat_w, att_src, att_dst, xp, a_src, a_dst, N);
-
-  hist_rank<<<1024, 256, 0, stream>>>(ei, E, N, cnt, erank);
-  if (E & 3) hist_rank_tail<<<1, 64, 0, stream>>>(ei, E, N, cnt, erank);
-  scan_local<<<NB, 1024, 0, stream>>>(cnt, row_ptr, blk_tot, N);
-  scan_apply2<<<NB, 1024, 0, stream>>>(row_ptr, blk_tot, N, NB);
-  fill_rank<<<1024, 256, 0, stream>>>(ei, E, N, row_ptr, erank, csr_src);
-  if (E & 3) fill_rank_tail<<<1, 64, 0, stream>>>(ei, E, N, row_ptr, erank, csr_src);
+  hipMemsetAsync(cnt, 0, (size_t)N * 4, stream);
+
+  K_front<<<ntXP + 64 + 1024, 256, 0, stream>>>(
+      x, gat_w, att_src, att_dst, xp, a_src, a_dst, N, ntXP,
+      pc_w, G, ei, E, N, cnt, erank);
+
+  K_scan<<<NB + 16, 1024, 0, stream>>>(cnt, row_ptr, blk_tot, N, NB, G, Hm);
+
+  K_apply<<<NB + 1, 256, 0, stream>>>(row_ptr, blk_tot, N, NB, Hm, sigma_inv);
+
+  K_fill<<<1024 + HID + 5, 256, 0, stream>>>(
+      ei, E, N, row_ptr, erank, csr_src,
+      pc_w, sigma_inv, mgf_w, mgf_b, sym_w, sym_b, out_w,
+      W1t, W2t, Wot, bias2);
 
   gat_aggregate<<<N, 64, 0, stream>>>(xp, a_src, a_dst, row_ptr, csr_src,
                                       gat_b, h_gat, N);
```
